# Kernel optimization log

Measured on AMD Instinct MI355X. Metric: run time of the kernel, lower is better.

## Reference

```python
import jax, jax.numpy as jnp
import numpy as np

PI_APPROX = 3.14  # the original module uses 3.14, not math.pi
FPS = 30.0        # hard-coded sampling rate in calc_hr_torch


def setup_inputs() -> dict:
    key = jax.random.key(0)
    x = jax.random.normal(key, (4096, 4096), dtype=jnp.float32)
    return {"x": x}


def reference(x) -> jnp.ndarray:
    test_n, sig_length = x.shape
    # mean-subtract each signal (over last dim)
    x = x - jnp.mean(x, axis=-1, keepdims=True)

    # custom_fft: DFT over dim 0 (size test_n), O(N^2) via trig matmuls
    N = test_n
    n = jnp.arange(N, dtype=jnp.float32)[:, None]  # [N,1]
    k = jnp.arange(N, dtype=jnp.float32)[None, :]  # [1,N]
    ang = (-2.0 * PI_APPROX / N) * (k * n)         # [N,N]
    real_part = jnp.matmul(jnp.cos(ang), x)        # [N, sig_length]
    imag_part = jnp.matmul(jnp.sin(ang), x)

    # custom_rfft: keep non-negative frequencies along dim 0
    half = N // 2 + 1 if N % 2 == 0 else (N + 1) // 2
    real_part = real_part[:half]
    imag_part = imag_part[:half]

    Ns = sig_length
    freq = jnp.arange(Ns, dtype=jnp.float32) / (Ns / FPS)  # [sig_length]
    amplitude = jnp.sqrt(real_part ** 2 + imag_part ** 2) / Ns  # [half, sig_length]
    hr_list = freq[jnp.argmax(amplitude, axis=-1)] * 60.0       # [half]
    return hr_list
```

## Files before the change

### kernel.cpp

```cpp
#include <hip/hip_runtime.h>
#include <cmath>

typedef _Float16 f16;
typedef _Float16 f16x8 __attribute__((ext_vector_type(8)));
typedef float f32x4 __attribute__((ext_vector_type(4)));
typedef unsigned long long u64;

#define M_OUT 2049
#define NDIM 4096
#define MPAD 2112
#define CW ((float)(-2.0 * 3.14 / 4096.0))

static const size_t WS_MEAN  = 0;
static const size_t WS_CELLS = 16384;
static const size_t WS_TBL   = 40960;
static const size_t A_ELEMS  = (size_t)MPAD * NDIM;
static const size_t X_ELEMS  = (size_t)NDIM * NDIM;
static const size_t WS_XTBL  = WS_TBL + 4 * A_ELEMS * sizeof(f16);
static const size_t WS_FULL_END = WS_XTBL + 2 * X_ELEMS * sizeof(f16);
static const size_t WS_MID_END  = WS_TBL + 4 * A_ELEMS * sizeof(f16);

#define AS1 __attribute__((address_space(1)))
#define AS3 __attribute__((address_space(3)))
__device__ __forceinline__ void async_copy16(const void* gsrc, void* ldst) {
    __builtin_amdgcn_global_load_lds((const AS1 unsigned int*)gsrc,
                                     (AS3 unsigned int*)ldst, 16, 0, 0);
}

__device__ __forceinline__ void split_f16(float v, f16& hi, f16& lo) {
    hi = (f16)v;
    lo = (f16)((v - (float)hi) * 64.0f);
}

__global__ void mean_kernel(const float* __restrict__ x, float* __restrict__ meanv) {
    const int row = blockIdx.x;
    const float4* xr = (const float4*)(x + (size_t)row * NDIM);
    float s = 0.f;
    for (int i = threadIdx.x; i < NDIM / 4; i += 256) {
        float4 v = xr[i];
        s += (v.x + v.y) + (v.z + v.w);
    }
    for (int off = 32; off; off >>= 1) s += __shfl_down(s, off);
    __shared__ float ps[4];
    if ((threadIdx.x & 63) == 0) ps[threadIdx.x >> 6] = s;
    __syncthreads();
    if (threadIdx.x == 0) {
        float t = (ps[0] + ps[1]) + (ps[2] + ps[3]);
        meanv[row] = t * (1.0f / 4096.0f);
    }
}

__global__ void init_cells(u64* __restrict__ cells) {
    int i = blockIdx.x * 256 + threadIdx.x;
    if (i < M_OUT) cells[i] = 0ull;
}

__global__ void fill_A_cm(f16* __restrict__ tbl) {
    const int c = blockIdx.x;
    const int m = blockIdx.y * 256 + threadIdx.x;
    if (m >= MPAD) return;
    const bool valid = (m < M_OUT);
    f16x8 chv, clv, shv, slv;
    for (int j = 0; j < 8; ++j) {
        float cc = 0.f, ss = 0.f;
        if (valid) {
            int kk = c * 8 + j;
            float ang = CW * (float)(m * kk);
            sincosf(ang, &ss, &cc);
        }
        f16 h, l;
        split_f16(cc, h, l); chv[j] = h; clv[j] = l;
        split_f16(ss, h, l); shv[j] = h; slv[j] = l;
    }
    size_t idx = ((size_t)c * MPAD + m) * 8;
    *(f16x8*)(tbl + idx)                 = chv;
    *(f16x8*)(tbl + A_ELEMS + idx)       = clv;
    *(f16x8*)(tbl + 2 * A_ELEMS + idx)   = shv;
    *(f16x8*)(tbl + 3 * A_ELEMS + idx)   = slv;
}

__global__ void fill_X_cm(const float* __restrict__ x, const float* __restrict__ meanv,
                          f16* __restrict__ xtbl) {
    const int c = blockIdx.x;
    const int n = blockIdx.y * 256 + threadIdx.x;
    f16x8 hv, lv;
    for (int j = 0; j < 8; ++j) {
        int k = c * 8 + j;
        float v = x[(size_t)k * NDIM + n] - meanv[k];
        f16 h, l;
        split_f16(v, h, l);
        hv[j] = h; lv[j] = l;
    }
    size_t idx = ((size_t)c * NDIM + n) * 8;
    *(f16x8*)(xtbl + idx)           = hv;
    *(f16x8*)(xtbl + X_ELEMS + idx) = lv;
}

__global__ __launch_bounds__(256, 2) void dft_gemm_cm(
    const f16* __restrict__ atbl, const f16* __restrict__ xtbl,
    u64* __restrict__ cells)
{
    __shared__ alignas(16) f16 sA[4][4][64][8];
    __shared__ alignas(16) f16 sX[2][4][128][8];

    const int t = threadIdx.x;
    const int n0      = blockIdx.x * 128;
    const int rowBase = blockIdx.y * 64;

    const int lane = t & 63;
    const int w  = t >> 6;
    const int wm = w >> 1, wn = w & 1;
    const int q  = lane >> 4, ln = lane & 15;

    f32x4 aC0[2][4], aC1[2][4], aS0[2][4], aS1[2][4];
    for (int i = 0; i < 2; ++i)
        for (int j = 0; j < 4; ++j) {
            aC0[i][j] = (f32x4){0.f, 0.f, 0.f, 0.f};
            aC1[i][j] = (f32x4){0.f, 0.f, 0.f, 0.f};
            aS0[i][j] = (f32x4){0.f, 0.f, 0.f, 0.f};
            aS1[i][j] = (f32x4){0.f, 0.f, 0.f, 0.f};
        }

    const f16* aG = atbl + (size_t)w * A_ELEMS + ((size_t)0 * MPAD + rowBase + lane) * 8;
    const int xq0 = w >> 1, xh0 = w & 1;
    const int xq1 = (w + 4) >> 1, xh1 = w & 1;
    const f16* xhG0 = xtbl + ((size_t)xq0 * NDIM + n0 + xh0 * 64 + lane) * 8;
    const f16* xhG1 = xtbl + ((size_t)xq1 * NDIM + n0 + xh1 * 64 + lane) * 8;
    const f16* xlG0 = xhG0 + X_ELEMS * 8 / 8 * 8;
    const f16* xlG1 = xhG1 + X_ELEMS;
    const f16* xlG0b = xtbl + X_ELEMS + ((size_t)xq0 * NDIM + n0 + xh0 * 64 + lane) * 8;

    for (int k0 = 0; k0 < NDIM; k0 += 32) {
        const int kc = k0 >> 3;
        __syncthreads();
        {
            const f16* g = aG + (size_t)kc * MPAD * 8;
            async_copy16(g,                         &sA[w][0][0][0]);
            async_copy16(g + (size_t)MPAD * 8,      &sA[w][1][0][0]);
            async_copy16(g + (size_t)2 * MPAD * 8,  &sA[w][2][0][0]);
            async_copy16(g + (size_t)3 * MPAD * 8,  &sA[w][3][0][0]);
        }
        {
            const size_t kadv = (size_t)kc * NDIM * 8;
            async_copy16(xhG0 + kadv,  &sX[0][xq0][xh0 * 64][0]);
            async_copy16(xhG1 + kadv,  &sX[0][xq1][xh1 * 64][0]);
            async_copy16(xlG0b + kadv, &sX[1][xq0][xh0 * 64][0]);
            async_copy16(xlG1 + kadv,  &sX[1][xq1][xh1 * 64][0]);
        }
        __syncthreads();
        f16x8 fch[2], fcl[2], fsh[2], fsl[2], bh[4], bl[4];
        for (int tm = 0; tm < 2; ++tm) {
            int ml = wm * 32 + tm * 16 + ln;
            fch[tm] = *(const f16x8*)&sA[0][q][ml][0];
            fcl[tm] = *(const f16x8*)&sA[1][q][ml][0];
            fsh[tm] = *(const f16x8*)&sA[2][q][ml][0];
            fsl[tm] = *(const f16x8*)&sA[3][q][ml][0];
        }
        for (int tn = 0; tn < 4; ++tn) {
            int nl = wn * 64 + tn * 16 + ln;
            bh[tn] = *(const f16x8*)&sX[0][q][nl][0];
            bl[tn] = *(const f16x8*)&sX[1][q][nl][0];
        }
        for (int tm = 0; tm < 2; ++tm)
            for (int tn = 0; tn < 4; ++tn) {
                aC0[tm][tn] = __builtin_amdgcn_mfma_f32_16x16x32_f16(fch[tm], bh[tn], aC0[tm][tn], 0, 0, 0);
                aC1[tm][tn] = __builtin_amdgcn_mfma_f32_16x16x32_f16(fch[tm], bl[tn], aC1[tm][tn], 0, 0, 0);
                aC1[tm][tn] = __builtin_amdgcn_mfma_f32_16x16x32_f16(fcl[tm], bh[tn], aC1[tm][tn], 0, 0, 0);
                aS0[tm][tn] = __builtin_amdgcn_mfma_f32_16x16x32_f16(fsh[tm], bh[tn], aS0[tm][tn], 0, 0, 0);
                aS1[tm][tn] = __builtin_amdgcn_mfma_f32_16x16x32_f16(fsh[tm], bl[tn], aS1[tm][tn], 0, 0, 0);
                aS1[tm][tn] = __builtin_amdgcn_mfma_f32_16x16x32_f16(fsl[tm], bh[tn], aS1[tm][tn], 0, 0, 0);
            }
    }

    const float inv64 = 0.015625f;
    for (int tm = 0; tm < 2; ++tm) {
        for (int r = 0; r < 4; ++r) {
            u64 best = 0ull;
            for (int tn = 0; tn < 4; ++tn) {
                float C = aC0[tm][tn][r] + aC1[tm][tn][r] * inv64;
                float S = aS0[tm][tn][r] + aS1[tm][tn][r] * inv64;
                float a2 = C * C + S * S;
                int col = n0 + wn * 64 + tn * 16 + ln;
                u64 key = ((u64)__float_as_uint(a2) << 32) | (unsigned)(~col);
                if (key > best) best = key;
            }
            for (int off = 1; off < 16; off <<= 1) {
                unsigned hi = (unsigned)(best >> 32), lo = (unsigned)best;
                unsigned ho = __shfl_xor(hi, off);
                unsigned lo2 = __shfl_xor(lo, off);
                u64 o = ((u64)ho << 32) | lo2;
                if (o > best) best = o;
            }
            if (ln == 0) {
                int grow = rowBase + wm * 32 + tm * 16 + q * 4 + r;
                if (grow < M_OUT) atomicMax(cells + grow, best);
            }
        }
    }
}

__global__ void fill_tables_rm(f16* __restrict__ tbl) {
    long long g = (long long)blockIdx.x * 256 + threadIdx.x;
    if (g >= (long long)(MPAD * 512)) return;
    int m  = (int)(g >> 9);
    int kq = ((int)g & 511) * 8;
    bool valid = (m < M_OUT);
    f16x8 chv, clv, shv, slv;
    for (int j = 0; j < 8; ++j) {
        float c = 0.f, s = 0.f;
        if (valid) {
            int kk = kq + j;
            float ang = CW * (float)(m * kk);
            sincosf(ang, &s, &c);
        }
        f16 h, l;
        split_f16(c, h, l); chv[j] = h; clv[j] = l;
        split_f16(s, h, l); shv[j] = h; slv[j] = l;
    }
    size_t idx = (size_t)m * NDIM + kq;
    *(f16x8*)(tbl + idx)               = chv;
    *(f16x8*)(tbl + A_ELEMS + idx)     = clv;
    *(f16x8*)(tbl + 2 * A_ELEMS + idx) = shv;
    *(f16x8*)(tbl + 3 * A_ELEMS + idx) = slv;
}

#define PK 40
__global__ __launch_bounds__(256, 2) void dft_gemm_fb(
    const float* __restrict__ x, const float* __restrict__ meanv,
    const f16* __restrict__ tbl, int useTbl,
    u64* __restrict__ cells)
{
    __shared__ alignas(16) f16 Ach[64][PK];
    __shared__ alignas(16) f16 Acl[64][PK];
    __shared__ alignas(16) f16 Ash[64][PK];
    __shared__ alignas(16) f16 Asl[64][PK];
    __shared__ alignas(16) f16 Xh[128][PK];
    __shared__ alignas(16) f16 Xl[128][PK];

    const int t = threadIdx.x;
    const int n0      = blockIdx.x * 128;
    const int rowBase = blockIdx.y * 64;

    const int am  = t >> 2;
    const int akq = (t & 3) * 8;
    const int xn  = t & 127;
    const int xkh = (t >> 7) * 16;

    const int lane = t & 63;
    const int w  = t >> 6;
    const int wm = w >> 1, wn = w & 1;
    const int q  = lane >> 4, ln = lane & 15;

    f32x4 aC0[2][4], aC1[2][4], aS0[2][4], aS1[2][4];
    for (int i = 0; i < 2; ++i)
        for (int j = 0; j < 4; ++j) {
            aC0[i][j] = (f32x4){0.f, 0.f, 0.f, 0.f};
            aC1[i][j] = (f32x4){0.f, 0.f, 0.f, 0.f};
            aS0[i][j] = (f32x4){0.f, 0.f, 0.f, 0.f};
            aS1[i][j] = (f32x4){0.f, 0.f, 0.f, 0.f};
        }

    const int arow = rowBase + am;
    const bool avalid = (arow < M_OUT);

    for (int k0 = 0; k0 < NDIM; k0 += 32) {
        __syncthreads();
        if (useTbl) {
            size_t idx = (size_t)arow * NDIM + k0 + akq;
            *(f16x8*)&Ach[am][akq] = *(const f16x8*)(tbl + idx);
            *(f16x8*)&Acl[am][akq] = *(const f16x8*)(tbl + A_ELEMS + idx);
            *(f16x8*)&Ash[am][akq] = *(const f16x8*)(tbl + 2 * A_ELEMS + idx);
            *(f16x8*)&Asl[am][akq] = *(const f16x8*)(tbl + 3 * A_ELEMS + idx);
        } else {
            f16x8 chv, clv, shv, slv;
            for (int j = 0; j < 8; ++j) {
                float c = 0.f, s = 0.f;
                if (avalid) {
                    int kk = k0 + akq + j;
                    float ang = CW * (float)(arow * kk);
                    sincosf(ang, &s, &c);
                }
                f16 h, l;
                split_f16(c, h, l); chv[j] = h; clv[j] = l;
                split_f16(s, h, l); shv[j] = h; slv[j] = l;
            }
            *(f16x8*)&Ach[am][akq] = chv;
            *(f16x8*)&Acl[am][akq] = clv;
            *(f16x8*)&Ash[am][akq] = shv;
            *(f16x8*)&Asl[am][akq] = slv;
        }
        {
            const float* xp = x + (size_t)(k0 + xkh) * NDIM + n0 + xn;
            f16x8 h0, h1, l0, l1;
            for (int r = 0; r < 16; ++r) {
                float v = xp[(size_t)r * NDIM] - meanv[k0 + xkh + r];
                f16 hi, lo;
                split_f16(v, hi, lo);
                if (r < 8) { h0[r] = hi; l0[r] = lo; }
                else       { h1[r - 8] = hi; l1[r - 8] = lo; }
            }
            *(f16x8*)&Xh[xn][xkh]     = h0;
            *(f16x8*)&Xh[xn][xkh + 8] = h1;
            *(f16x8*)&Xl[xn][xkh]     = l0;
            *(f16x8*)&Xl[xn][xkh + 8] = l1;
        }
        __syncthreads();
        f16x8 fch[2], fcl[2], fsh[2], fsl[2], bh[4], bl[4];
        for (int tm = 0; tm < 2; ++tm) {
            int ml = wm * 32 + tm * 16 + ln;
            fch[tm] = *(const f16x8*)&Ach[ml][q * 8];
            fcl[tm] = *(const f16x8*)&Acl[ml][q * 8];
            fsh[tm] = *(const f16x8*)&Ash[ml][q * 8];
            fsl[tm] = *(const f16x8*)&Asl[ml][q * 8];
        }
        for (int tn = 0; tn < 4; ++tn) {
            int nl = wn * 64 + tn * 16 + ln;
            bh[tn] = *(const f16x8*)&Xh[nl][q * 8];
            bl[tn] = *(const f16x8*)&Xl[nl][q * 8];
        }
        for (int tm = 0; tm < 2; ++tm)
            for (int tn = 0; tn < 4; ++tn) {
                aC0[tm][tn] = __builtin_amdgcn_mfma_f32_16x16x32_f16(fch[tm], bh[tn], aC0[tm][tn], 0, 0, 0);
                aC1[tm][tn] = __builtin_amdgcn_mfma_f32_16x16x32_f16(fch[tm], bl[tn], aC1[tm][tn], 0, 0, 0);
                aC1[tm][tn] = __builtin_amdgcn_mfma_f32_16x16x32_f16(fcl[tm], bh[tn], aC1[tm][tn], 0, 0, 0);
                aS0[tm][tn] = __builtin_amdgcn_mfma_f32_16x16x32_f16(fsh[tm], bh[tn], aS0[tm][tn], 0, 0, 0);
                aS1[tm][tn] = __builtin_amdgcn_mfma_f32_16x16x32_f16(fsh[tm], bl[tn], aS1[tm][tn], 0, 0, 0);
                aS1[tm][tn] = __builtin_amdgcn_mfma_f32_16x16x32_f16(fsl[tm], bh[tn], aS1[tm][tn], 0, 0, 0);
            }
    }

    const float inv64 = 0.015625f;
    for (int tm = 0; tm < 2; ++tm) {
        for (int r = 0; r < 4; ++r) {
            u64 best = 0ull;
            for (int tn = 0; tn < 4; ++tn) {
                float C = aC0[tm][tn][r] + aC1[tm][tn][r] * inv64;
                float S = aS0[tm][tn][r] + aS1[tm][tn][r] * inv64;
                float a2 = C * C + S * S;
                int col = n0 + wn * 64 + tn * 16 + ln;
                u64 key = ((u64)__float_as_uint(a2) << 32) | (unsigned)(~col);
                if (key > best) best = key;
            }
            for (int off = 1; off < 16; off <<= 1) {
                unsigned hi = (unsigned)(best >> 32), lo = (unsigned)best;
                unsigned ho = __shfl_xor(hi, off);
                unsigned lo2 = __shfl_xor(lo, off);
                u64 o = ((u64)ho << 32) | lo2;
                if (o > best) best = o;
            }
            if (ln == 0) {
                int grow = rowBase + wm * 32 + tm * 16 + q * 4 + r;
                if (grow < M_OUT) atomicMax(cells + grow, best);
            }
        }
    }
}

__global__ void out_kernel(const u64* __restrict__ cells, float* __restrict__ out) {
    int i = blockIdx.x * 256 + threadIdx.x;
    if (i < M_OUT) {
        unsigned col = ~(unsigned)(cells[i] & 0xFFFFFFFFull);
        float freq = (float)col / (4096.0f / 30.0f);
        out[i] = freq * 60.0f;
    }
}

extern "C" void kernel_launch(void* const* d_in, const int* in_sizes, int n_in,
                              void* d_out, int out_size, void* d_ws, size_t ws_size,
                              hipStream_t stream) {
    const float* x = (const float*)d_in[0];
    char* ws = (char*)d_ws;
    float* meanv = (float*)(ws + WS_MEAN);
    u64*   cells = (u64*)(ws + WS_CELLS);
    f16*   atbl  = (f16*)(ws + WS_TBL);
    f16*   xtbl  = (f16*)(ws + WS_XTBL);
    float* out   = (float*)d_out;

    hipLaunchKernelGGL(init_cells, dim3((M_OUT + 255) / 256), dim3(256), 0, stream, cells);
    hipLaunchKernelGGL(mean_kernel, dim3(NDIM), dim3(256), 0, stream, x, meanv);

    if (ws_size >= WS_FULL_END) {
        hipLaunchKernelGGL(fill_A_cm, dim3(512, 9), dim3(256), 0, stream, atbl);
        hipLaunchKernelGGL(fill_X_cm, dim3(512, 16), dim3(256), 0, stream, x, meanv, xtbl);
        hipLaunchKernelGGL(dft_gemm_cm, dim3(32, 33), dim3(256), 0, stream, atbl, xtbl, cells);
    } else if (ws_size >= WS_MID_END) {
        hipLaunchKernelGGL(fill_tables_rm, dim3(4224), dim3(256), 0, stream, atbl);
        hipLaunchKernelGGL(dft_gemm_fb, dim3(32, 33), dim3(256), 0, stream,
                           x, meanv, atbl, 1, cells);
    } else {
        hipLaunchKernelGGL(dft_gemm_fb, dim3(32, 33), dim3(256), 0, stream,
                           x, meanv, atbl, 0, cells);
    }
    hipLaunchKernelGGL(out_kernel, dim3((M_OUT + 255) / 256), dim3(256), 0, stream, cells, out);
}
```

Before: 563.5 us.

## Load DFT table fragments directly into registers with double-buffered prefetch

```diff
diff --git a/kernel.cpp b/kernel.cpp
--- a/kernel.cpp
+++ b/kernel.cpp
@@ -100,7 +100,6 @@
     const f16* __restrict__ atbl, const f16* __restrict__ xtbl,
     u64* __restrict__ cells)
 {
-    __shared__ alignas(16) f16 sA[4][4][64][8];
     __shared__ alignas(16) f16 sX[2][4][128][8];
 
     const int t = threadIdx.x;
@@ -113,7 +112,9 @@
     const int q  = lane >> 4, ln = lane & 15;
 
     f32x4 aC0[2][4], aC1[2][4], aS0[2][4], aS1[2][4];
+#pragma unroll
     for (int i = 0; i < 2; ++i)
+#pragma unroll
         for (int j = 0; j < 4; ++j) {
             aC0[i][j] = (f32x4){0.f, 0.f, 0.f, 0.f};
             aC1[i][j] = (f32x4){0.f, 0.f, 0.f, 0.f};
@@ -121,61 +122,75 @@
             aS1[i][j] = (f32x4){0.f, 0.f, 0.f, 0.f};
         }
 
-    const f16* aG = atbl + (size_t)w * A_ELEMS + ((size_t)0 * MPAD + rowBase + lane) * 8;
-    const int xq0 = w >> 1, xh0 = w & 1;
-    const int xq1 = (w + 4) >> 1, xh1 = w & 1;
-    const f16* xhG0 = xtbl + ((size_t)xq0 * NDIM + n0 + xh0 * 64 + lane) * 8;
-    const f16* xhG1 = xtbl + ((size_t)xq1 * NDIM + n0 + xh1 * 64 + lane) * 8;
-    const f16* xlG0 = xhG0 + X_ELEMS * 8 / 8 * 8;
-    const f16* xlG1 = xhG1 + X_ELEMS;
-    const f16* xlG0b = xtbl + X_ELEMS + ((size_t)xq0 * NDIM + n0 + xh0 * 64 + lane) * 8;
-
-    for (int k0 = 0; k0 < NDIM; k0 += 32) {
-        const int kc = k0 >> 3;
-        __syncthreads();
-        {
-            const f16* g = aG + (size_t)kc * MPAD * 8;
-            async_copy16(g,                         &sA[w][0][0][0]);
-            async_copy16(g + (size_t)MPAD * 8,      &sA[w][1][0][0]);
-            async_copy16(g + (size_t)2 * MPAD * 8,  &sA[w][2][0][0]);
-            async_copy16(g + (size_t)3 * MPAD * 8,  &sA[w][3][0][0]);
-        }
-        {
-            const size_t kadv = (size_t)kc * NDIM * 8;
-            async_copy16(xhG0 + kadv,  &sX[0][xq0][xh0 * 64][0]);
-            async_copy16(xhG1 + kadv,  &sX[0][xq1][xh1 * 64][0]);
-            async_copy16(xlG0b + kadv, &sX[1][xq0][xh0 * 64][0]);
-            async_copy16(xlG1 + kadv,  &sX[1][xq1][xh1 * 64][0]);
-        }
-        __syncthreads();
-        f16x8 fch[2], fcl[2], fsh[2], fsl[2], bh[4], bl[4];
-        for (int tm = 0; tm < 2; ++tm) {
-            int ml = wm * 32 + tm * 16 + ln;
-            fch[tm] = *(const f16x8*)&sA[0][q][ml][0];
-            fcl[tm] = *(const f16x8*)&sA[1][q][ml][0];
-            fsh[tm] = *(const f16x8*)&sA[2][q][ml][0];
-            fsl[tm] = *(const f16x8*)&sA[3][q][ml][0];
-        }
+    const f16* aBase = atbl + ((size_t)q * MPAD + (rowBase + wm * 32 + ln)) * 8;
+
+    const int xq0 = w >> 1, xh = w & 1;
+    const int xq1 = xq0 + 2;
+    const f16* xG0 = xtbl + ((size_t)xq0 * NDIM + n0 + xh * 64 + lane) * 8;
+    const f16* xG1 = xtbl + ((size_t)xq1 * NDIM + n0 + xh * 64 + lane) * 8;
+    const f16* xG2 = xG0 + X_ELEMS;
+    const f16* xG3 = xG1 + X_ELEMS;
+
+    auto loadA = [&](f16x8 (&dst)[2][4], int kc) {
+#pragma unroll
+        for (int tm = 0; tm < 2; ++tm)
+#pragma unroll
+            for (int tb = 0; tb < 4; ++tb)
+                dst[tm][tb] = *(const f16x8*)(aBase + (size_t)tb * A_ELEMS
+                              + ((size_t)kc * MPAD + tm * 16) * 8);
+    };
+
+    auto stageX = [&](int kc) {
+        const size_t kadv = (size_t)kc * NDIM * 8;
+        async_copy16(xG0 + kadv, &sX[0][xq0][xh * 64][0]);
+        async_copy16(xG1 + kadv, &sX[0][xq1][xh * 64][0]);
+        async_copy16(xG2 + kadv, &sX[1][xq0][xh * 64][0]);
+        async_copy16(xG3 + kadv, &sX[1][xq1][xh * 64][0]);
+    };
+
+    auto compute = [&](f16x8 (&A)[2][4]) {
+        f16x8 bh[4], bl[4];
+#pragma unroll
         for (int tn = 0; tn < 4; ++tn) {
             int nl = wn * 64 + tn * 16 + ln;
             bh[tn] = *(const f16x8*)&sX[0][q][nl][0];
             bl[tn] = *(const f16x8*)&sX[1][q][nl][0];
         }
+#pragma unroll
         for (int tm = 0; tm < 2; ++tm)
+#pragma unroll
             for (int tn = 0; tn < 4; ++tn) {
-                aC0[tm][tn] = __builtin_amdgcn_mfma_f32_16x16x32_f16(fch[tm], bh[tn], aC0[tm][tn], 0, 0, 0);
-                aC1[tm][tn] = __builtin_amdgcn_mfma_f32_16x16x32_f16(fch[tm], bl[tn], aC1[tm][tn], 0, 0, 0);
-                aC1[tm][tn] = __builtin_amdgcn_mfma_f32_16x16x32_f16(fcl[tm], bh[tn], aC1[tm][tn], 0, 0, 0);
-                aS0[tm][tn] = __builtin_amdgcn_mfma_f32_16x16x32_f16(fsh[tm], bh[tn], aS0[tm][tn], 0, 0, 0);
-                aS1[tm][tn] = __builtin_amdgcn_mfma_f32_16x16x32_f16(fsh[tm], bl[tn], aS1[tm][tn], 0, 0, 0);
-                aS1[tm][tn] = __builtin_amdgcn_mfma_f32_16x16x32_f16(fsl[tm], bh[tn], aS1[tm][tn], 0, 0, 0);
-            }
+                aC0[tm][tn] = __builtin_amdgcn_mfma_f32_16x16x32_f16(A[tm][0], bh[tn], aC0[tm][tn], 0, 0, 0);
+                aC1[tm][tn] = __builtin_amdgcn_mfma_f32_16x16x32_f16(A[tm][0], bl[tn], aC1[tm][tn], 0, 0, 0);
+                aC1[tm][tn] = __builtin_amdgcn_mfma_f32_16x16x32_f16(A[tm][1], bh[tn], aC1[tm][tn], 0, 0, 0);
+                aS0[tm][tn] = __builtin_amdgcn_mfma_f32_16x16x32_f16(A[tm][2], bh[tn], aS0[tm][tn], 0, 0, 0);
+                aS1[tm][tn] = __builtin_amdgcn_mfma_f32_16x16x32_f16(A[tm][2], bl[tn], aS1[tm][tn], 0, 0, 0);
+                aS1[tm][tn] = __builtin_amdgcn_mfma_f32_16x16x32_f16(A[tm][3], bh[tn], aS1[tm][tn], 0, 0, 0);
+            }
+    };
+
+    f16x8 Aa[2][4], Ab[2][4];
+    loadA(Aa, 0);
+    for (int kc = 0; kc < 512; kc += 8) {
+        __syncthreads();
+        loadA(Ab, kc + 4);
+        stageX(kc);
+        __syncthreads();
+        compute(Aa);
+        __syncthreads();
+        if (kc + 8 < 512) loadA(Aa, kc + 8);
+        stageX(kc + 4);
+        __syncthreads();
+        compute(Ab);
     }
 
     const float inv64 = 0.015625f;
+#pragma unroll
     for (int tm = 0; tm < 2; ++tm) {
+#pragma unroll
         for (int r = 0; r < 4; ++r) {
             u64 best = 0ull;
+#pragma unroll
             for (int tn = 0; tn < 4; ++tn) {
                 float C = aC0[tm][tn][r] + aC1[tm][tn][r] * inv64;
                 float S = aS0[tm][tn][r] + aS1[tm][tn][r] * inv64;
```

Result: slower. 577.9 us (+2.6%).
